# Kernel optimization log

Hardware: AMD Instinct MI355X
Metric: run time of the kernel (lower is better)

Reference implementation:

```python
import jax, jax.numpy as jnp
import numpy as np

N_NODES = 100000
N_EDGES = 600000
D_IN = 128
D_OUT = 128

def gcn_conv(x, src, dst, W, b, n):
    # PyG GCNConv: h = X W; out_i = sum_j norm_ij * h_j + b, with self-loops and
    # symmetric normalization norm_ij = deg_i^{-1/2} deg_j^{-1/2}.
    deg = jax.ops.segment_sum(jnp.ones_like(dst, dtype=x.dtype), dst, num_segments=n)
    dinv = jnp.where(deg > 0, jax.lax.rsqrt(deg), 0.0)
    norm = dinv[src] * dinv[dst]            # [E]
    h = x @ W                                # [N, D_out]
    msg = h[src] * norm[:, None]             # gather + scale, [E, D_out]
    out = jax.ops.segment_sum(msg, dst, num_segments=n)
    return out + b

def setup_inputs() -> dict:
    key = jax.random.key(0)
    ks = jax.random.split(key, 8)
    x = jax.random.normal(ks[0], (N_NODES, D_IN), dtype=jnp.float32)
    edge_index = jax.random.randint(ks[1], (2, N_EDGES), 0, N_NODES, dtype=jnp.int64)
    s = (1.0 / np.sqrt(D_IN)).astype(np.float32) if isinstance(np.sqrt(D_IN), np.ndarray) else np.float32(1.0 / np.sqrt(D_IN))
    W1 = jax.random.normal(ks[2], (D_IN, D_OUT), dtype=jnp.float32) * s
    b1 = jnp.zeros((D_OUT,), dtype=jnp.float32)
    W2 = jax.random.normal(ks[3], (D_OUT, D_OUT), dtype=jnp.float32) * np.float32(1.0 / np.sqrt(D_OUT))
    b2 = jnp.zeros((D_OUT,), dtype=jnp.float32)
    Wfc = jax.random.normal(ks[4], (D_IN, D_OUT), dtype=jnp.float32) * s
    bfc = jnp.zeros((D_OUT,), dtype=jnp.float32)
    return {"x": x, "edge_index": edge_index, "W1": W1, "b1": b1,
            "W2": W2, "b2": b2, "Wfc": Wfc, "bfc": bfc}

def reference(x, edge_index, W1, b1, W2, b2, Wfc, bfc):
    n = x.shape[0]
    loop = jnp.arange(n, dtype=edge_index.dtype)
    src = jnp.concatenate([edge_index[0], loop])  # add self-loops
    dst = jnp.concatenate([edge_index[1], loop])
    res = x @ Wfc + bfc                           # linear residual branch
    h = jax.nn.relu(gcn_conv(x, src, dst, W1, b1, n))
    h = jax.nn.relu(gcn_conv(h, src, dst, W2, b2, n))
    return h + res
```

## Files before the change

### kernel.cpp

```cpp
#include <hip/hip_runtime.h>
#include <hip/hip_bf16.h>

#define D 128

typedef __bf16 bf16x8 __attribute__((ext_vector_type(8)));
typedef float f32x16 __attribute__((ext_vector_type(16)));

union U16 { uint4 u; bf16x8 v; };

static __device__ __forceinline__ unsigned short f2bf(float f) {
    unsigned u = __float_as_uint(f);
    unsigned r = (u + 0x7fffu + ((u >> 16) & 1u)) >> 16;
    return (unsigned short)r;
}
static __device__ __forceinline__ float bf2f(unsigned short s) {
    return __uint_as_float(((unsigned)s) << 16);
}
static __device__ __forceinline__ float u2f_lo(unsigned x) { return __uint_as_float(x << 16); }
static __device__ __forceinline__ float u2f_hi(unsigned x) { return __uint_as_float(x & 0xffff0000u); }

__global__ __launch_bounds__(256) void k_prep(
        const float* __restrict__ W1, const float* __restrict__ W2, const float* __restrict__ Wf,
        unsigned short* __restrict__ W1h, unsigned short* __restrict__ W1l,
        unsigned short* __restrict__ W2h, unsigned short* __restrict__ W2l,
        unsigned short* __restrict__ Wfh, unsigned short* __restrict__ Wfl,
        int* __restrict__ cnt, int n) {
    int idx = blockIdx.x * 256 + threadIdx.x;
    if (idx < 3 * 16384) {
        int which = idx >> 14;
        int local = idx & 16383;
        int k = local >> 7, c = local & 127;
        const float* W = (which == 0) ? W1 : (which == 1) ? W2 : Wf;
        unsigned short* Wh = (which == 0) ? W1h : (which == 1) ? W2h : Wfh;
        unsigned short* Wl = (which == 0) ? W1l : (which == 1) ? W2l : Wfl;
        float v = W[k * 128 + c];
        unsigned short h = f2bf(v);
        unsigned short l = f2bf(v - bf2f(h));
        Wh[c * 128 + k] = h;
        Wl[c * 128 + k] = l;
    }
    if (idx < n) cnt[idx] = 0;
}


__global__ __launch_bounds__(256) void k_hist(const int* __restrict__ dst,
                                              int* __restrict__ cnt, int e) {
    int i = blockIdx.x * 256 + threadIdx.x;
    if (i < e) atomicAdd(&cnt[dst[i]], 1);
}

#define SCAN_CHUNK 1024

__global__ __launch_bounds__(256) void k_scan_local(const int* __restrict__ cnt,
                                                    int* __restrict__ ptr,
                                                    int* __restrict__ sums, int n) {
    __shared__ int tsum[256];
    const int t = threadIdx.x;
    const int base = blockIdx.x * SCAN_CHUNK + t * 4;
    int v[4]; int s = 0;
    #pragma unroll
    for (int i = 0; i < 4; ++i) {
        int idx = base + i;
        v[i] = (idx < n) ? cnt[idx] : 0;
        s += v[i];
    }
    tsum[t] = s;
    __syncthreads();
    for (int off = 1; off < 256; off <<= 1) {
        int x = (t >= off) ? tsum[t - off] : 0;
        __syncthreads();
        tsum[t] += x;
        __syncthreads();
    }
    int run = (t > 0) ? tsum[t - 1] : 0;
    if (t == 255) sums[blockIdx.x] = tsum[255];
    #pragma unroll
    for (int i = 0; i < 4; ++i) {
        int idx = base + i;
        if (idx < n) ptr[idx] = run;
        run += v[i];
    }
}

__global__ __launch_bounds__(256) void k_scan_sums(int* __restrict__ sums, int nChunks) {
    __shared__ int ls[256];
    const int t = threadIdx.x;
    ls[t] = (t < nChunks) ? sums[t] : 0;
    __syncthreads();
    for (int off = 1; off < 256; off <<= 1) {
        int x = (t >= off) ? ls[t - off] : 0;
        __syncthreads();
        ls[t] += x;
        __syncthreads();
    }
    if (t < nChunks) sums[t] = (t > 0) ? ls[t - 1] : 0;
}

__global__ __launch_bounds__(256) void k_scan_add(int* __restrict__ ptr,
                                                  const int* __restrict__ sums,
                                                  int* __restrict__ cnt,
                                                  float* __restrict__ dinv,
                                                  int n, int e) {
    int i = blockIdx.x * 256 + threadIdx.x;
    if (i < n) {
        ptr[i] += sums[i >> 10];
        dinv[i] = rsqrtf((float)(1 + cnt[i]));
        cnt[i] = 0;
    }
    if (i == 0) ptr[n] = e;
}

__global__ __launch_bounds__(256) void k_fill(const int* __restrict__ src,
                                              const int* __restrict__ dst,
                                              const int* __restrict__ ptr,
                                              int* __restrict__ fill,
                                              const float* __restrict__ dinv,
                                              uint2* __restrict__ csr, int e) {
    int i = blockIdx.x * 256 + threadIdx.x;
    if (i < e) {
        int d = dst[i];
        int s = src[i];
        int slot = ptr[d] + atomicAdd(&fill[d], 1);
        csr[slot] = make_uint2((unsigned)s, __float_as_uint(dinv[s]));
    }
}

#define APAD 136

__global__ __launch_bounds__(512, 4) void k_gemm_dual(
        const float* __restrict__ A,
        const unsigned short* __restrict__ B1h, const unsigned short* __restrict__ B1l,
        const unsigned short* __restrict__ B2h, const unsigned short* __restrict__ B2l,
        const float* __restrict__ bias2,
        unsigned short* __restrict__ out1,
        float* __restrict__ out2,
        int M, int nTiles) {
    __shared__ __align__(16) unsigned short As[2][32][APAD];

    const int tid = threadIdx.x;
    const int wave = tid >> 6;
    const int lane = tid & 63;
    const int l31 = lane & 31;
    const int quad8 = (lane >> 5) * 8;
    const int col = (wave & 3) * 32 + l31;
    const int sel = wave >> 2;

    const unsigned short* __restrict__ Bh = sel ? B2h : B1h;
    const unsigned short* __restrict__ Bl = sel ? B2l : B1l;

    U16 bh[8], bl[8];
    #pragma unroll
    for (int ks = 0; ks < 8; ++ks) {
        const size_t bo = (size_t)col * D + ks * 16 + quad8;
        bh[ks].u = *(const uint4*)(Bh + bo);
        bl[ks].u = *(const uint4*)(Bl + bo);
    }
    const float bv = bias2[col];

    for (int t = blockIdx.x; t < nTiles; t += gridDim.x) {
        const int row0 = t * 32;

        #pragma unroll
        for (int i = 0; i < 2; ++i) {
            int f = tid + i * 512;
            int r = f >> 5, c4 = (f & 31) * 4;
            int rg = row0 + r; if (rg >= M) rg = M - 1;
            float4 v = *(const float4*)(A + (size_t)rg * D + c4);
            ushort4 hq, lq;
            hq.x = f2bf(v.x); hq.y = f2bf(v.y); hq.z = f2bf(v.z); hq.w = f2bf(v.w);
            lq.x = f2bf(v.x - bf2f(hq.x)); lq.y = f2bf(v.y - bf2f(hq.y));
            lq.z = f2bf(v.z - bf2f(hq.z)); lq.w = f2bf(v.w - bf2f(hq.w));
            *(ushort4*)&As[0][r][c4] = hq;
            *(ushort4*)&As[1][r][c4] = lq;
        }
        __syncthreads();

        f32x16 acc;
        #pragma unroll
        for (int r = 0; r < 16; ++r) acc[r] = 0.f;

        #pragma unroll
        for (int ks = 0; ks < 8; ++ks) {
            U16 ah, al;
            ah.u = *(const uint4*)&As[0][l31][ks * 16 + quad8];
            al.u = *(const uint4*)&As[1][l31][ks * 16 + quad8];
            acc = __builtin_amdgcn_mfma_f32_32x32x16_bf16(ah.v, bh[ks].v, acc, 0, 0, 0);
            acc = __builtin_amdgcn_mfma_f32_32x32x16_bf16(ah.v, bl[ks].v, acc, 0, 0, 0);
            acc = __builtin_amdgcn_mfma_f32_32x32x16_bf16(al.v, bh[ks].v, acc, 0, 0, 0);
        }
        __syncthreads();

        if (sel == 0) {
            #pragma unroll
            for (int reg = 0; reg < 16; ++reg) {
                const int r = (reg & 3) + 8 * (reg >> 2) + 4 * (lane >> 5);
                const int rg = row0 + r;
                if (rg < M) out1[(size_t)rg * D + col] = f2bf(acc[reg]);
            }
        } else {
            #pragma unroll
            for (int reg = 0; reg < 16; ++reg) {
                const int r = (reg & 3) + 8 * (reg >> 2) + 4 * (lane >> 5);
                const int rg = row0 + r;
                if (rg < M) out2[(size_t)rg * D + col] = acc[reg] + bv;
            }
        }
    }
}

__global__ __launch_bounds__(256, 4) void k_gemm_rr_bf(
        const unsigned short* __restrict__ A,
        const unsigned short* __restrict__ Bh, const unsigned short* __restrict__ Bl,
        unsigned short* __restrict__ outb,
        int M, int nTiles) {
    __shared__ __align__(16) unsigned short As[32][APAD];

    const int tid = threadIdx.x;
    const int wave = tid >> 6;
    const int lane = tid & 63;
    const int l31 = lane & 31;
    const int quad8 = (lane >> 5) * 8;
    const int col = wave * 32 + l31;

    U16 bh[8], bl[8];
    #pragma unroll
    for (int ks = 0; ks < 8; ++ks) {
        const size_t bo = (size_t)col * D + ks * 16 + quad8;
        bh[ks].u = *(const uint4*)(Bh + bo);
        bl[ks].u = *(const uint4*)(Bl + bo);
    }

    for (int t = blockIdx.x; t < nTiles; t += gridDim.x) {
        const int row0 = t * 32;

        #pragma unroll
        for (int i = 0; i < 2; ++i) {
            int f = tid + i * 256;
            int r = f >> 4, c8 = (f & 15) * 8;
            int rg = row0 + r; if (rg >= M) rg = M - 1;
            *(uint4*)&As[r][c8] = *(const uint4*)(A + (size_t)rg * D + c8);
        }
        __syncthreads();

        f32x16 acc;
        #pragma unroll
        for (int r = 0; r < 16; ++r) acc[r] = 0.f;

        #pragma unroll
        for (int ks = 0; ks < 8; ++ks) {
            U16 ah;
            ah.u = *(const uint4*)&As[l31][ks * 16 + quad8];
            acc = __builtin_amdgcn_mfma_f32_32x32x16_bf16(ah.v, bh[ks].v, acc, 0, 0, 0);
            acc = __builtin_amdgcn_mfma_f32_32x32x16_bf16(ah.v, bl[ks].v, acc, 0, 0, 0);
        }
        __syncthreads();

        #pragma unroll
        for (int reg = 0; reg < 16; ++reg) {
            const int r = (reg & 3) + 8 * (reg >> 2) + 4 * (lane >> 5);
            const int rg = row0 + r;
            if (rg < M) outb[(size_t)rg * D + col] = f2bf(acc[reg]);
        }
    }
}

__global__ __launch_bounds__(256) void k_gather_w(const int* __restrict__ ptr,
                                                  const uint2* __restrict__ csr,
                                                  const float* __restrict__ dinv,
                                                  const unsigned short* __restrict__ h,
                                                  const float* __restrict__ bias,
                                                  const float* __restrict__ res,
                                                  float* __restrict__ outf,
                                                  unsigned short* __restrict__ outb,
                                                  int N) {
    const int g = threadIdx.x >> 5;
    const int lane = threadIdx.x & 31;
    const int i = blockIdx.x * 8 + g;
    if (i >= N) return;

    const int p0 = ptr[i];
    const int p1 = ptr[i + 1];
    const float di = dinv[i];

    const uint2 us = *(const uint2*)(h + (size_t)i * D + lane * 4);
    const float4 bvv = *(const float4*)(bias + lane * 4);

    float a0 = 0.f, a1 = 0.f, a2 = 0.f, a3 = 0.f;
    const unsigned* cb = (const unsigned*)csr;
    int j = p0;
    for (; j + 4 <= p1; j += 4) {
        const uint4 e0 = *(const uint4*)(cb + 2 * (size_t)j);
        const uint4 e1 = *(const uint4*)(cb + 2 * (size_t)j + 4);
        const float c0 = __uint_as_float(e0.y);
        const float c1 = __uint_as_float(e0.w);
        const float c2 = __uint_as_float(e1.y);
        const float c3 = __uint_as_float(e1.w);
        const uint2 u0 = *(const uint2*)(h + (size_t)e0.x * D + lane * 4);
        const uint2 u1 = *(const uint2*)(h + (size_t)e0.z * D + lane * 4);
        const uint2 u2 = *(const uint2*)(h + (size_t)e1.x * D + lane * 4);
        const uint2 u3 = *(const uint2*)(h + (size_t)e1.z * D + lane * 4);
        a0 = fmaf(c0, u2f_lo(u0.x), a0); a1 = fmaf(c0, u2f_hi(u0.x), a1);
        a2 = fmaf(c0, u2f_lo(u0.y), a2); a3 = fmaf(c0, u2f_hi(u0.y), a3);
        a0 = fmaf(c1, u2f_lo(u1.x), a0); a1 = fmaf(c1, u2f_hi(u1.x), a1);
        a2 = fmaf(c1, u2f_lo(u1.y), a2); a3 = fmaf(c1, u2f_hi(u1.y), a3);
        a0 = fmaf(c2, u2f_lo(u2.x), a0); a1 = fmaf(c2, u2f_hi(u2.x), a1);
        a2 = fmaf(c2, u2f_lo(u2.y), a2); a3 = fmaf(c2, u2f_hi(u2.y), a3);
        a0 = fmaf(c3, u2f_lo(u3.x), a0); a1 = fmaf(c3, u2f_hi(u3.x), a1);
        a2 = fmaf(c3, u2f_lo(u3.y), a2); a3 = fmaf(c3, u2f_hi(u3.y), a3);
    }
    const int r = p1 - j;
    if (r > 0) {
        const int j1 = (r > 1) ? j + 1 : j;
        const int j2 = (r > 2) ? j + 2 : j;
        const uint2 e0 = csr[j];
        const uint2 e1 = csr[j1];
        const uint2 e2 = csr[j2];
        const float c0 = __uint_as_float(e0.y);
        const float c1 = (r > 1) ? __uint_as_float(e1.y) : 0.f;
        const float c2 = (r > 2) ? __uint_as_float(e2.y) : 0.f;
        const uint2 u0 = *(const uint2*)(h + (size_t)e0.x * D + lane * 4);
        const uint2 u1 = *(const uint2*)(h + (size_t)e1.x * D + lane * 4);
        const uint2 u2 = *(const uint2*)(h + (size_t)e2.x * D + lane * 4);
        a0 = fmaf(c0, u2f_lo(u0.x), a0); a1 = fmaf(c0, u2f_hi(u0.x), a1);
        a2 = fmaf(c0, u2f_lo(u0.y), a2); a3 = fmaf(c0, u2f_hi(u0.y), a3);
        a0 = fmaf(c1, u2f_lo(u1.x), a0); a1 = fmaf(c1, u2f_hi(u1.x), a1);
        a2 = fmaf(c1, u2f_lo(u1.y), a2); a3 = fmaf(c1, u2f_hi(u1.y), a3);
        a0 = fmaf(c2, u2f_lo(u2.x), a0); a1 = fmaf(c2, u2f_hi(u2.x), a1);
        a2 = fmaf(c2, u2f_lo(u2.y), a2); a3 = fmaf(c2, u2f_hi(u2.y), a3);
    }

    const float self = di * di;
    float o0 = fmaxf(di * a0 + self * u2f_lo(us.x) + bvv.x, 0.0f);
    float o1 = fmaxf(di * a1 + self * u2f_hi(us.x) + bvv.y, 0.0f);
    float o2 = fmaxf(di * a2 + self * u2f_lo(us.y) + bvv.z, 0.0f);
    float o3 = fmaxf(di * a3 + self * u2f_hi(us.y) + bvv.w, 0.0f);
    if (outb) {
        ushort4 q = {f2bf(o0), f2bf(o1), f2bf(o2), f2bf(o3)};
        *(ushort4*)(outb + (size_t)i * D + lane * 4) = q;
    } else {
        const float4 rv = *(const float4*)(res + (size_t)i * D + lane * 4);
        float4 o = {o0 + rv.x, o1 + rv.y, o2 + rv.z, o3 + rv.w};
        *(float4*)(outf + (size_t)i * D + lane * 4) = o;
    }
}


extern "C" void kernel_launch(void* const* d_in, const int* in_sizes, int n_in,
                              void* d_out, int out_size, void* d_ws, size_t ws_size,
                              hipStream_t stream) {
    const int N = in_sizes[0] / D;
    const int E = in_sizes[1] / 2;

    const float* x   = (const float*)d_in[0];
    const int*   ei  = (const int*)d_in[1];
    const int*   src = ei;
    const int*   dst = ei + E;
    const float* W1  = (const float*)d_in[2];
    const float* b1  = (const float*)d_in[3];
    const float* W2  = (const float*)d_in[4];
    const float* b2  = (const float*)d_in[5];
    const float* Wfc = (const float*)d_in[6];
    const float* bfc = (const float*)d_in[7];
    float* out = (float*)d_out;

    char* ws = (char*)d_ws;
    size_t off = 0;
    auto alloc = [&](size_t bytes) { char* p = ws + off; off += (bytes + 255) & ~(size_t)255; return p; };
    float* dinv    = (float*)alloc((size_t)N * 4);
    int*   cnt     = (int*)  alloc((size_t)N * 4);
    int*   ptr     = (int*)  alloc((size_t)(N + 1) * 4);
    int*   sums    = (int*)  alloc(256 * 4);
    uint2* csr     = (uint2*)alloc((size_t)(E + 64) * sizeof(uint2));
    unsigned short* W1h = (unsigned short*)alloc(128 * 128 * 2);
    unsigned short* W1l = (unsigned short*)alloc(128 * 128 * 2);
    unsigned short* W2h = (unsigned short*)alloc(128 * 128 * 2);
    unsigned short* W2l = (unsigned short*)alloc(128 * 128 * 2);
    unsigned short* Wfh = (unsigned short*)alloc(128 * 128 * 2);
    unsigned short* Wfl = (unsigned short*)alloc(128 * 128 * 2);
    unsigned short* h    = (unsigned short*)alloc((size_t)N * D * 2);
    unsigned short* hb16 = (unsigned short*)alloc((size_t)N * D * 2);

    const int nBlk    = (N + 255) / 256;
    const int eBlk    = (E + 255) / 256;
    const int aBlk    = (N + 7) / 8;
    const int nChunks = (N + SCAN_CHUNK - 1) / SCAN_CHUNK;
    const int nTiles  = (N + 31) / 32;
    const int gBlk    = nTiles < 1024 ? nTiles : 1024;
    const int pBlk    = (nBlk > 192) ? nBlk : 192;

    k_prep<<<pBlk, 256, 0, stream>>>(W1, W2, Wfc, W1h, W1l, W2h, W2l, Wfh, Wfl, cnt, N);

    k_hist<<<eBlk, 256, 0, stream>>>(dst, cnt, E);
    k_scan_local<<<nChunks, 256, 0, stream>>>(cnt, ptr, sums, N);
    k_scan_sums<<<1, 256, 0, stream>>>(sums, nChunks);
    k_scan_add<<<nBlk, 256, 0, stream>>>(ptr, sums, cnt, dinv, N, E);
    k_fill<<<eBlk, 256, 0, stream>>>(src, dst, ptr, cnt, dinv, csr, E);

    k_gemm_dual<<<gBlk, 512, 0, stream>>>(x, W1h, W1l, Wfh, Wfl, bfc, h, out, N, nTiles);

    k_gather_w<<<aBlk, 256, 0, stream>>>(ptr, csr, dinv, h, b1, nullptr, nullptr, hb16, N);

    k_gemm_rr_bf<<<gBlk, 256, 0, stream>>>(hb16, W2h, W2l, h, N, nTiles);

    k_gather_w<<<aBlk, 256, 0, stream>>>(ptr, csr, dinv, h, b2, out, out, nullptr, N);
}
```

Measured before the change: 294.0 us.

## Fuse layer-1 aggregation into layer-2 GEMM and double-buffer dual GEMM A tiles

Layer-1 neighbour aggregation (gather, normalize, bias, ReLU, bf16 convert) now runs inside the second GEMM kernel and writes each 32-row tile straight into shared memory. This removes the intermediate bf16 activation buffer's write and read and one kernel launch. The dual GEMM also gains a double-buffered shared tile with register prefetch of the next A tile, and one of its __syncthreads is dropped. The risk is that the fused kernel's gather has lower parallelism (8 groups of 32 threads each handling 4 rows per tile, with a grid capped at 1024 blocks), which could make the latency-bound gather slower than the standalone gather kernel.

```diff
diff --git a/kernel.cpp b/kernel.cpp
--- a/kernel.cpp
+++ b/kernel.cpp
@@ -135,7 +135,7 @@
         unsigned short* __restrict__ out1,
         float* __restrict__ out2,
         int M, int nTiles) {
-    __shared__ __align__(16) unsigned short As[2][32][APAD];
+    __shared__ __align__(16) unsigned short As[2][2][32][APAD];
 
     const int tid = threadIdx.x;
     const int wave = tid >> 6;
@@ -157,22 +157,45 @@
     }
     const float bv = bias2[col];
 
-    for (int t = blockIdx.x; t < nTiles; t += gridDim.x) {
+    const int r0 = tid >> 5;
+    const int c0 = (tid & 31) * 4;
+    const int r1 = r0 + 16;
+
+    int t = blockIdx.x;
+    float4 v0, v1;
+    if (t < nTiles) {
+        int rg0 = t * 32 + r0; if (rg0 >= M) rg0 = M - 1;
+        int rg1 = t * 32 + r1; if (rg1 >= M) rg1 = M - 1;
+        v0 = *(const float4*)(A + (size_t)rg0 * D + c0);
+        v1 = *(const float4*)(A + (size_t)rg1 * D + c0);
+    }
+    int cur = 0;
+
+    while (t < nTiles) {
         const int row0 = t * 32;
 
-        #pragma unroll
-        for (int i = 0; i < 2; ++i) {
-            int f = tid + i * 512;
-            int r = f >> 5, c4 = (f & 31) * 4;
-            int rg = row0 + r; if (rg >= M) rg = M - 1;
-            float4 v = *(const float4*)(A + (size_t)rg * D + c4);
+        {
             ushort4 hq, lq;
-            hq.x = f2bf(v.x); hq.y = f2bf(v.y); hq.z = f2bf(v.z); hq.w = f2bf(v.w);
-            lq.x = f2bf(v.x - bf2f(hq.x)); lq.y = f2bf(v.y - bf2f(hq.y));
-            lq.z = f2bf(v.z - bf2f(hq.z)); lq.w = f2bf(v.w - bf2f(hq.w));
-            *(ushort4*)&As[0][r][c4] = hq;
-            *(ushort4*)&As[1][r][c4] = lq;
-        }
+            hq.x = f2bf(v0.x); hq.y = f2bf(v0.y); hq.z = f2bf(v0.z); hq.w = f2bf(v0.w);
+            lq.x = f2bf(v0.x - bf2f(hq.x)); lq.y = f2bf(v0.y - bf2f(hq.y));
+            lq.z = f2bf(v0.z - bf2f(hq.z)); lq.w = f2bf(v0.w - bf2f(hq.w));
+            *(ushort4*)&As[cur][0][r0][c0] = hq;
+            *(ushort4*)&As[cur][1][r0][c0] = lq;
+            hq.x = f2bf(v1.x); hq.y = f2bf(v1.y); hq.z = f2bf(v1.z); hq.w = f2bf(v1.w);
+            lq.x = f2bf(v1.x - bf2f(hq.x)); lq.y = f2bf(v1.y - bf2f(hq.y));
+            lq.z = f2bf(v1.z - bf2f(hq.z)); lq.w = f2bf(v1.w - bf2f(hq.w));
+            *(ushort4*)&As[cur][0][r1][c0] = hq;
+            *(ushort4*)&As[cur][1][r1][c0] = lq;
+        }
+
+        const int tn = t + gridDim.x;
+        if (tn < nTiles) {
+            int rg0 = tn * 32 + r0; if (rg0 >= M) rg0 = M - 1;
+            int rg1 = tn * 32 + r1; if (rg1 >= M) rg1 = M - 1;
+            v0 = *(const float4*)(A + (size_t)rg0 * D + c0);
+            v1 = *(const float4*)(A + (size_t)rg1 * D + c0);
+        }
+
         __syncthreads();
 
         f32x16 acc;
@@ -182,13 +205,12 @@
         #pragma unroll
         for (int ks = 0; ks < 8; ++ks) {
             U16 ah, al;
-            ah.u = *(const uint4*)&As[0][l31][ks * 16 + quad8];
-            al.u = *(const uint4*)&As[1][l31][ks * 16 + quad8];
+            ah.u = *(const uint4*)&As[cur][0][l31][ks * 16 + quad8];
+            al.u = *(const uint4*)&As[cur][1][l31][ks * 16 + quad8];
             acc = __builtin_amdgcn_mfma_f32_32x32x16_bf16(ah.v, bh[ks].v, acc, 0, 0, 0);
             acc = __builtin_amdgcn_mfma_f32_32x32x16_bf16(ah.v, bl[ks].v, acc, 0, 0, 0);
             acc = __builtin_amdgcn_mfma_f32_32x32x16_bf16(al.v, bh[ks].v, acc, 0, 0, 0);
         }
-        __syncthreads();
 
         if (sel == 0) {
             #pragma unroll
@@ -205,11 +227,18 @@
                 if (rg < M) out2[(size_t)rg * D + col] = acc[reg] + bv;
             }
         }
-    }
-}
-
-__global__ __launch_bounds__(256, 4) void k_gemm_rr_bf(
-        const unsigned short* __restrict__ A,
+
+        cur ^= 1;
+        t = tn;
+    }
+}
+
+__global__ __launch_bounds__(256, 4) void k_agg_gemm(
+        const int* __restrict__ ptr,
+        const uint2* __restrict__ csr,
+        const float* __restrict__ dinv,
+        const unsigned short* __restrict__ h,
+        const float* __restrict__ bias,
         const unsigned short* __restrict__ Bh, const unsigned short* __restrict__ Bl,
         unsigned short* __restrict__ outb,
         int M, int nTiles) {
@@ -217,10 +246,13 @@
 
     const int tid = threadIdx.x;
     const int wave = tid >> 6;
-    const int lane = tid & 63;
-    const int l31 = lane & 31;
-    const int quad8 = (lane >> 5) * 8;
+    const int lane64 = tid & 63;
+    const int l31 = lane64 & 31;
+    const int quad8 = (lane64 >> 5) * 8;
     const int col = wave * 32 + l31;
+
+    const int g = tid >> 5;
+    const int lane = tid & 31;
 
     U16 bh[8], bl[8];
     #pragma unroll
@@ -229,16 +261,70 @@
         bh[ks].u = *(const uint4*)(Bh + bo);
         bl[ks].u = *(const uint4*)(Bl + bo);
     }
+    const float4 bvv = *(const float4*)(bias + lane * 4);
+    const unsigned* cb = (const unsigned*)csr;
 
     for (int t = blockIdx.x; t < nTiles; t += gridDim.x) {
         const int row0 = t * 32;
 
-        #pragma unroll
-        for (int i = 0; i < 2; ++i) {
-            int f = tid + i * 256;
-            int r = f >> 4, c8 = (f & 15) * 8;
-            int rg = row0 + r; if (rg >= M) rg = M - 1;
-            *(uint4*)&As[r][c8] = *(const uint4*)(A + (size_t)rg * D + c8);
+        for (int rr = 0; rr < 4; ++rr) {
+            const int r = g * 4 + rr;
+            int ig = row0 + r; if (ig >= M) ig = M - 1;
+            const int p0 = ptr[ig];
+            const int p1 = ptr[ig + 1];
+            const float di = dinv[ig];
+            const uint2 us = *(const uint2*)(h + (size_t)ig * D + lane * 4);
+
+            float a0 = 0.f, a1 = 0.f, a2 = 0.f, a3 = 0.f;
+            int j = p0;
+            for (; j + 4 <= p1; j += 4) {
+                const uint4 e0 = *(const uint4*)(cb + 2 * (size_t)j);
+                const uint4 e1 = *(const uint4*)(cb + 2 * (size_t)j + 4);
+                const float c0 = __uint_as_float(e0.y);
+                const float c1 = __uint_as_float(e0.w);
+                const float c2 = __uint_as_float(e1.y);
+                const float c3 = __uint_as_float(e1.w);
+                const uint2 u0 = *(const uint2*)(h + (size_t)e0.x * D + lane * 4);
+                const uint2 u1 = *(const uint2*)(h + (size_t)e0.z * D + lane * 4);
+                const uint2 u2 = *(const uint2*)(h + (size_t)e1.x * D + lane * 4);
+                const uint2 u3 = *(const uint2*)(h + (size_t)e1.z * D + lane * 4);
+                a0 = fmaf(c0, u2f_lo(u0.x), a0); a1 = fmaf(c0, u2f_hi(u0.x), a1);
+                a2 = fmaf(c0, u2f_lo(u0.y), a2); a3 = fmaf(c0, u2f_hi(u0.y), a3);
+                a0 = fmaf(c1, u2f_lo(u1.x), a0); a1 = fmaf(c1, u2f_hi(u1.x), a1);
+                a2 = fmaf(c1, u2f_lo(u1.y), a2); a3 = fmaf(c1, u2f_hi(u1.y), a3);
+                a0 = fmaf(c2, u2f_lo(u2.x), a0); a1 = fmaf(c2, u2f_hi(u2.x), a1);
+                a2 = fmaf(c2, u2f_lo(u2.y), a2); a3 = fmaf(c2, u2f_hi(u2.y), a3);
+                a0 = fmaf(c3, u2f_lo(u3.x), a0); a1 = fmaf(c3, u2f_hi(u3.x), a1);
+                a2 = fmaf(c3, u2f_lo(u3.y), a2); a3 = fmaf(c3, u2f_hi(u3.y), a3);
+            }
+            const int rem = p1 - j;
+            if (rem > 0) {
+                const int j1 = (rem > 1) ? j + 1 : j;
+                const int j2 = (rem > 2) ? j + 2 : j;
+                const uint2 e0 = csr[j];
+                const uint2 e1 = csr[j1];
+                const uint2 e2 = csr[j2];
+                const float c0 = __uint_as_float(e0.y);
+                const float c1 = (rem > 1) ? __uint_as_float(e1.y) : 0.f;
+                const float c2 = (rem > 2) ? __uint_as_float(e2.y) : 0.f;
+                const uint2 u0 = *(const uint2*)(h + (size_t)e0.x * D + lane * 4);
+                const uint2 u1 = *(const uint2*)(h + (size_t)e1.x * D + lane * 4);
+                const uint2 u2 = *(const uint2*)(h + (size_t)e2.x * D + lane * 4);
+                a0 = fmaf(c0, u2f_lo(u0.x), a0); a1 = fmaf(c0, u2f_hi(u0.x), a1);
+                a2 = fmaf(c0, u2f_lo(u0.y), a2); a3 = fmaf(c0, u2f_hi(u0.y), a3);
+                a0 = fmaf(c1, u2f_lo(u1.x), a0); a1 = fmaf(c1, u2f_hi(u1.x), a1);
+                a2 = fmaf(c1, u2f_lo(u1.y), a2); a3 = fmaf(c1, u2f_hi(u1.y), a3);
+                a0 = fmaf(c2, u2f_lo(u2.x), a0); a1 = fmaf(c2, u2f_hi(u2.x), a1);
+                a2 = fmaf(c2, u2f_lo(u2.y), a2); a3 = fmaf(c2, u2f_hi(u2.y), a3);
+            }
+
+            const float self = di * di;
+            const float o0 = fmaxf(di * a0 + self * u2f_lo(us.x) + bvv.x, 0.0f);
+            const float o1 = fmaxf(di * a1 + self * u2f_hi(us.x) + bvv.y, 0.0f);
+            const float o2 = fmaxf(di * a2 + self * u2f_lo(us.y) + bvv.z, 0.0f);
+            const float o3 = fmaxf(di * a3 + self * u2f_hi(us.y) + bvv.w, 0.0f);
+            ushort4 q = {f2bf(o0), f2bf(o1), f2bf(o2), f2bf(o3)};
+            *(ushort4*)&As[r][lane * 4] = q;
         }
         __syncthreads();
 
@@ -257,7 +343,7 @@
 
         #pragma unroll
         for (int reg = 0; reg < 16; ++reg) {
-            const int r = (reg & 3) + 8 * (reg >> 2) + 4 * (lane >> 5);
+            const int r = (reg & 3) + 8 * (reg >> 2) + 4 * (lane64 >> 5);
             const int rg = row0 + r;
             if (rg < M) outb[(size_t)rg * D + col] = f2bf(acc[reg]);
         }
@@ -377,8 +463,8 @@
     unsigned short* W2l = (unsigned short*)alloc(128 * 128 * 2);
     unsigned short* Wfh = (unsigned short*)alloc(128 * 128 * 2);
     unsigned short* Wfl = (unsigned short*)alloc(128 * 128 * 2);
-    unsigned short* h    = (unsigned short*)alloc((size_t)N * D * 2);
-    unsigned short* hb16 = (unsigned short*)alloc((size_t)N * D * 2);
+    unsigned short* h   = (unsigned short*)alloc((size_t)N * D * 2);
+    unsigned short* h2  = (unsigned short*)alloc((size_t)N * D * 2);
 
     const int nBlk    = (N + 255) / 256;
     const int eBlk    = (E + 255) / 256;
@@ -398,9 +484,7 @@
 
     k_gemm_dual<<<gBlk, 512, 0, stream>>>(x, W1h, W1l, Wfh, Wfl, bfc, h, out, N, nTiles);
 
-    k_gather_w<<<aBlk, 256, 0, stream>>>(ptr, csr, dinv, h, b1, nullptr, nullptr, hb16, N);
-
-    k_gemm_rr_bf<<<gBlk, 256, 0, stream>>>(hb16, W2h, W2l, h, N, nTiles);
-
-    k_gather_w<<<aBlk, 256, 0, stream>>>(ptr, csr, dinv, h, b2, out, out, nullptr, N);
-}
+    k_agg_gemm<<<gBlk, 256, 0, stream>>>(ptr, csr, dinv, h, b1, W2h, W2l, h2, N, nTiles);
+
+    k_gather_w<<<aBlk, 256, 0, stream>>>(ptr, csr, dinv, h2, b2, out, out, nullptr, N);
+}
```

New measurement: 290.2 us. Within noise of the previous version (-1.3%).
